# Kernel tuning notes

Hardware: AMD Instinct MI355X
Metric: run time of the kernel (lower is better)

The kernel has to match this reference:

```python
import jax, jax.numpy as jnp
import numpy as np

EPS = 1e-8  # torch CosineSimilarity default eps


def setup_inputs() -> dict:
    key = jax.random.key(0)
    k_emb, k_idx, k_w1, k_w2 = jax.random.split(key, 4)
    N, H, E = 50000, 128, 800000
    emb = jax.random.normal(k_emb, (N, H), dtype=jnp.float32)
    edge_index = jax.random.randint(k_idx, (2, E), 0, N, dtype=jnp.int64)
    # xavier_uniform for square H x H: limit = sqrt(6 / (H + H))
    lim = float(np.sqrt(6.0 / (H + H)))
    W1 = jax.random.uniform(k_w1, (H, H), dtype=jnp.float32, minval=-lim, maxval=lim)
    W2 = jax.random.uniform(k_w2, (H, H), dtype=jnp.float32, minval=-lim, maxval=lim)
    b1 = jnp.zeros((H,), dtype=jnp.float32)
    b2 = jnp.zeros((H,), dtype=jnp.float32)
    return {"emb": emb, "edge_index": edge_index, "W1": W1, "b1": b1, "W2": W2, "b2": b2}


def reference(emb, edge_index, W1, b1, W2, b2):
    col, row = edge_index[0], edge_index[1]

    def mlp(x):  # Linear -> (Dropout: identity at eval) -> ELU -> Linear
        h = jax.nn.elu(x @ W1.T + b1)
        return h @ W2.T + b2

    f1 = mlp(emb[col])  # [E, H]
    f2 = mlp(emb[row])  # [E, H]
    n1 = jnp.maximum(jnp.sqrt(jnp.sum(f1 * f1, axis=1)), EPS)
    n2 = jnp.maximum(jnp.sqrt(jnp.sum(f2 * f2, axis=1)), EPS)
    return jnp.sum(f1 * f2, axis=1) / (n1 * n2)  # [E]
```

## Files before the change

kernel.cpp:

```cpp
#include <hip/hip_runtime.h>
#include <math.h>

#define H 128
#define MROWS 64
#define XS 136

typedef __attribute__((ext_vector_type(8))) short short8;
typedef __attribute__((ext_vector_type(4))) float floatx4;

__device__ __forceinline__ unsigned short f2bf(float f) {
    unsigned u = __float_as_uint(f);
    return (unsigned short)((u + 0x7FFFu + ((u >> 16) & 1u)) >> 16);
}

__global__ void prep_weights(const float* __restrict__ W1,
                             const float* __restrict__ W2,
                             unsigned short* __restrict__ Wbf) {
    int i = blockIdx.x * 256 + threadIdx.x;
    if (i < 16384)       Wbf[i] = f2bf(W1[i]);
    else if (i < 32768)  Wbf[i] = f2bf(W2[i - 16384]);
}

__global__ __launch_bounds__(256, 2) void mlp_mfma(
    const float* __restrict__ emb, const unsigned short* __restrict__ Wbf,
    const float* __restrict__ b1, const float* __restrict__ b2,
    signed char* __restrict__ qtab, float* __restrict__ scl, int N)
{
    __shared__ unsigned short Wl[H * XS];
    __shared__ char dbuf[2 * MROWS * XS * 2];
    __shared__ float invn_s[MROWS];
    __shared__ float amax_s[MROWS];

    unsigned short* xs = (unsigned short*)dbuf;
    unsigned short* hs = xs + MROWS * XS;
    float*          gs = (float*)dbuf;

    const int tid   = threadIdx.x;
    const int wave  = tid >> 6, lane = tid & 63;
    const int quad  = lane >> 4, l15 = lane & 15;
    const int node0 = blockIdx.x * MROWS;

    {
        const float4* src = (const float4*)Wbf;
        #pragma unroll
        for (int i = 0; i < 8; ++i) {
            int cc = i * 256 + tid;
            int row = cc >> 4, c = cc & 15;
            *(float4*)(Wl + row * XS + c * 8) = src[cc];
        }
    }
    #pragma unroll
    for (int i = 0; i < 8; ++i) {
        int flat = i * 1024 + tid * 4;
        int rowl = flat >> 7, col = flat & 127;
        float4 v = make_float4(0.f, 0.f, 0.f, 0.f);
        if (node0 + rowl < N)
            v = *(const float4*)(emb + (size_t)(node0 + rowl) * H + col);
        ushort4 b;
        b.x = f2bf(v.x); b.y = f2bf(v.y); b.z = f2bf(v.z); b.w = f2bf(v.w);
        *(ushort4*)(xs + rowl * XS + col) = b;
    }
    __syncthreads();

    short8 afr[4];
    const int mrow = wave * 16 + l15;

    #pragma unroll
    for (int ks = 0; ks < 4; ++ks)
        afr[ks] = *(const short8*)(xs + mrow * XS + ks * 32 + quad * 8);
    #pragma unroll
    for (int nt = 0; nt < 8; ++nt) {
        floatx4 acc = {0.f, 0.f, 0.f, 0.f};
        #pragma unroll
        for (int ks = 0; ks < 4; ++ks) {
            short8 bfr = *(const short8*)(Wl + (nt * 16 + l15) * XS + ks * 32 + quad * 8);
            acc = __builtin_amdgcn_mfma_f32_16x16x32_bf16(afr[ks], bfr, acc, 0, 0, 0);
        }
        const int col = nt * 16 + l15;
        const float bb = b1[col];
        #pragma unroll
        for (int r = 0; r < 4; ++r) {
            float v = acc[r] + bb;
            v = v > 0.f ? v : (__expf(v) - 1.f);
            hs[(wave * 16 + quad * 4 + r) * XS + col] = f2bf(v);
        }
    }
    __syncthreads();

    {
        const float4* src = (const float4*)(Wbf + 16384);
        #pragma unroll
        for (int i = 0; i < 8; ++i) {
            int cc = i * 256 + tid;
            int row = cc >> 4, c = cc & 15;
            *(float4*)(Wl + row * XS + c * 8) = src[cc];
        }
    }
    __syncthreads();

    #pragma unroll
    for (int ks = 0; ks < 4; ++ks)
        afr[ks] = *(const short8*)(hs + mrow * XS + ks * 32 + quad * 8);
    __syncthreads();

    float sq[4] = {0.f, 0.f, 0.f, 0.f};
    float am[4] = {0.f, 0.f, 0.f, 0.f};
    #pragma unroll
    for (int nt = 0; nt < 8; ++nt) {
        floatx4 acc = {0.f, 0.f, 0.f, 0.f};
        #pragma unroll
        for (int ks = 0; ks < 4; ++ks) {
            short8 bfr = *(const short8*)(Wl + (nt * 16 + l15) * XS + ks * 32 + quad * 8);
            acc = __builtin_amdgcn_mfma_f32_16x16x32_bf16(afr[ks], bfr, acc, 0, 0, 0);
        }
        const int col = nt * 16 + l15;
        const float bb = b2[col];
        #pragma unroll
        for (int r = 0; r < 4; ++r) {
            float v = acc[r] + bb;
            gs[(wave * 16 + quad * 4 + r) * H + col] = v;
            sq[r] += v * v;
            am[r] = fmaxf(am[r], fabsf(v));
        }
    }
    #pragma unroll
    for (int r = 0; r < 4; ++r) {
        float s = sq[r], a = am[r];
        #pragma unroll
        for (int m = 8; m; m >>= 1) {
            s += __shfl_xor(s, m);
            a = fmaxf(a, __shfl_xor(a, m));
        }
        if (l15 == 0) {
            const int row = wave * 16 + quad * 4 + r;
            float nn = sqrtf(s);
            if (nn < 1e-8f) nn = 1e-8f;
            invn_s[row] = 1.f / nn;
            amax_s[row] = fmaxf(a, 1e-20f);
        }
    }
    __syncthreads();

    if (tid < MROWS && node0 + tid < N)
        scl[node0 + tid] = amax_s[tid] * invn_s[tid] * (1.f / 127.f);

    #pragma unroll
    for (int i = 0; i < 2; ++i) {
        int chunk = i * 256 + tid;
        int row = chunk >> 3, c0 = (chunk & 7) * 16;
        if (node0 + row < N) {
            const float qs = 127.f / amax_s[row];
            unsigned u[4];
            #pragma unroll
            for (int w = 0; w < 4; ++w) {
                unsigned pk = 0;
                #pragma unroll
                for (int j = 0; j < 4; ++j) {
                    float v = gs[row * H + c0 + w * 4 + j] * qs;
                    int q = (int)rintf(v);
                    q = q > 127 ? 127 : (q < -127 ? -127 : q);
                    pk |= ((unsigned)(q & 255)) << (8 * j);
                }
                u[w] = pk;
            }
            *(uint4*)(qtab + (size_t)(node0 + row) * H + c0) =
                make_uint4(u[0], u[1], u[2], u[3]);
        }
    }
}

__device__ __forceinline__ int dot4(unsigned a, unsigned b) {
    int s = 0;
    #pragma unroll
    for (int j = 0; j < 4; ++j)
        s += (int)((signed char)(a >> (8 * j))) * (int)((signed char)(b >> (8 * j)));
    return s;
}

__global__ __launch_bounds__(256) void edge_cos(
    const int* __restrict__ ei, const signed char* __restrict__ qtab,
    const float* __restrict__ scl, float* __restrict__ out, int E)
{
    const int gid = blockIdx.x * 256 + threadIdx.x;
    const int e = gid >> 3, sub = gid & 7;
    if (e >= E) return;

    const int c = ei[e];
    const int r = ei[e + E];

    const uint4 ua = *(const uint4*)(qtab + (size_t)c * H + sub * 16);
    const uint4 ub = *(const uint4*)(qtab + (size_t)r * H + sub * 16);
    int s = dot4(ua.x, ub.x) + dot4(ua.y, ub.y)
          + dot4(ua.z, ub.z) + dot4(ua.w, ub.w);

    #pragma unroll
    for (int m = 4; m; m >>= 1) s += __shfl_xor(s, m);
    if (sub == 0) out[e] = (float)s * scl[c] * scl[r];
}

extern "C" void kernel_launch(void* const* d_in, const int* in_sizes, int n_in,
                              void* d_out, int out_size, void* d_ws, size_t ws_size,
                              hipStream_t stream) {
    const float* emb = (const float*)d_in[0];
    const int*   ei  = (const int*)d_in[1];
    const float* W1  = (const float*)d_in[2];
    const float* b1  = (const float*)d_in[3];
    const float* W2  = (const float*)d_in[4];
    const float* b2  = (const float*)d_in[5];
    float*       out = (float*)d_out;

    const int N = in_sizes[0] / H;
    const int E = in_sizes[1] / 2;

    unsigned short* Wbf  = (unsigned short*)d_ws;
    signed char*    qtab = (signed char*)(Wbf + 32768);
    float*          scl  = (float*)(qtab + (size_t)N * H);

    prep_weights<<<128, 256, 0, stream>>>(W1, W2, Wbf);
    mlp_mfma<<<(N + MROWS - 1) / MROWS, 256, 0, stream>>>(emb, Wbf, b1, b2, qtab, scl, N);
    edge_cos<<<(E * 8 + 255) / 256, 256, 0, stream>>>(ei, qtab, scl, out, E);
}
```

Before: 123.5 us.

## Bucket edges by endpoint node range for XCD-local gathers; quantize from registers

Adds histogram, scan and scatter kernels that sort edges into 8x8 buckets by source and destination node range, storing packed (c, r) pairs with the original edge index. The edge kernel then assigns each source bucket to blocks congruent modulo 8, so gathers from the int8 table stay within a smaller slice per cache domain. The MLP epilogue now quantizes directly from accumulator registers instead of staging through shared memory, using a permuted column layout that leaves the dot product unchanged. The cost is extra passes over edge_index, scattered list writes and three more launches, and node ids are packed into 16 bits, which assumes N < 65536.

```diff
diff --git a/kernel.cpp b/kernel.cpp
--- a/kernel.cpp
+++ b/kernel.cpp
@@ -4,6 +4,8 @@
 #define H 128
 #define MROWS 64
 #define XS 136
+#define NB 8
+#define NB2 64
 
 typedef __attribute__((ext_vector_type(8))) short short8;
 typedef __attribute__((ext_vector_type(4))) float floatx4;
@@ -13,12 +15,71 @@
     return (unsigned short)((u + 0x7FFFu + ((u >> 16) & 1u)) >> 16);
 }
 
+__device__ __forceinline__ int bkt(int c, float s8) {
+    int b = (int)((float)c * s8);
+    return b > (NB - 1) ? (NB - 1) : b;
+}
+
 __global__ void prep_weights(const float* __restrict__ W1,
                              const float* __restrict__ W2,
-                             unsigned short* __restrict__ Wbf) {
+                             unsigned short* __restrict__ Wbf,
+                             unsigned* __restrict__ cnt) {
+    if (blockIdx.x == 0 && threadIdx.x < NB2) cnt[threadIdx.x] = 0;
     int i = blockIdx.x * 256 + threadIdx.x;
     if (i < 16384)       Wbf[i] = f2bf(W1[i]);
     else if (i < 32768)  Wbf[i] = f2bf(W2[i - 16384]);
+}
+
+__global__ __launch_bounds__(256) void hist_k(const int* __restrict__ ei, int E,
+                                              float s8, unsigned* __restrict__ cnt) {
+    __shared__ unsigned h[NB2];
+    if (threadIdx.x < NB2) h[threadIdx.x] = 0;
+    __syncthreads();
+    const int stride = gridDim.x * 256;
+    for (int e = blockIdx.x * 256 + threadIdx.x; e < E; e += stride) {
+        int c = ei[e], r = ei[e + E];
+        atomicAdd(&h[bkt(c, s8) * NB + bkt(r, s8)], 1u);
+    }
+    __syncthreads();
+    if (threadIdx.x < NB2 && h[threadIdx.x])
+        atomicAdd(&cnt[threadIdx.x], h[threadIdx.x]);
+}
+
+__global__ void scan_k(const unsigned* __restrict__ cnt,
+                       unsigned* __restrict__ bb, unsigned* __restrict__ cur) {
+    if (threadIdx.x == 0) {
+        unsigned acc = 0;
+        for (int i = 0; i < NB2; ++i) { bb[i] = acc; cur[i] = acc; acc += cnt[i]; }
+        bb[NB2] = acc;
+    }
+}
+
+__global__ __launch_bounds__(256) void scatter_k(const int* __restrict__ ei, int E,
+                                                 float s8, unsigned* __restrict__ cur,
+                                                 uint2* __restrict__ lst) {
+    __shared__ unsigned h[NB2];
+    __shared__ unsigned base_s[NB2];
+    const int nchunk = (E + 255) >> 8;
+    for (int ch = blockIdx.x; ch < nchunk; ch += gridDim.x) {
+        if (threadIdx.x < NB2) h[threadIdx.x] = 0;
+        __syncthreads();
+        const int e = ch * 256 + threadIdx.x;
+        const bool v = e < E;
+        int c = 0, r = 0, b = 0; unsigned rank = 0;
+        if (v) {
+            c = ei[e]; r = ei[e + E];
+            b = bkt(c, s8) * NB + bkt(r, s8);
+            rank = atomicAdd(&h[b], 1u);
+        }
+        __syncthreads();
+        if (threadIdx.x < NB2 && h[threadIdx.x])
+            base_s[threadIdx.x] = atomicAdd(&cur[threadIdx.x], h[threadIdx.x]);
+        __syncthreads();
+        if (v)
+            lst[base_s[b] + rank] =
+                make_uint2((unsigned)c | ((unsigned)r << 16), (unsigned)e);
+        __syncthreads();
+    }
 }
 
 __global__ __launch_bounds__(256, 2) void mlp_mfma(
@@ -27,13 +88,8 @@
     signed char* __restrict__ qtab, float* __restrict__ scl, int N)
 {
     __shared__ unsigned short Wl[H * XS];
-    __shared__ char dbuf[2 * MROWS * XS * 2];
-    __shared__ float invn_s[MROWS];
-    __shared__ float amax_s[MROWS];
-
-    unsigned short* xs = (unsigned short*)dbuf;
-    unsigned short* hs = xs + MROWS * XS;
-    float*          gs = (float*)dbuf;
+    __shared__ unsigned short xs[MROWS * XS];
+    __shared__ unsigned short hs[MROWS * XS];
 
     const int tid   = threadIdx.x;
     const int wave  = tid >> 6, lane = tid & 63;
@@ -62,8 +118,8 @@
     }
     __syncthreads();
 
+    const int mrow = wave * 16 + l15;
     short8 afr[4];
-    const int mrow = wave * 16 + l15;
 
     #pragma unroll
     for (int ks = 0; ks < 4; ++ks)
@@ -77,16 +133,19 @@
             acc = __builtin_amdgcn_mfma_f32_16x16x32_bf16(afr[ks], bfr, acc, 0, 0, 0);
         }
         const int col = nt * 16 + l15;
-        const float bb = b1[col];
+        const float bb1 = b1[col];
         #pragma unroll
         for (int r = 0; r < 4; ++r) {
-            float v = acc[r] + bb;
+            float v = acc[r] + bb1;
             v = v > 0.f ? v : (__expf(v) - 1.f);
             hs[(wave * 16 + quad * 4 + r) * XS + col] = f2bf(v);
         }
     }
     __syncthreads();
 
+    #pragma unroll
+    for (int ks = 0; ks < 4; ++ks)
+        afr[ks] = *(const short8*)(hs + mrow * XS + ks * 32 + quad * 8);
     {
         const float4* src = (const float4*)(Wbf + 16384);
         #pragma unroll
@@ -98,11 +157,7 @@
     }
     __syncthreads();
 
-    #pragma unroll
-    for (int ks = 0; ks < 4; ++ks)
-        afr[ks] = *(const short8*)(hs + mrow * XS + ks * 32 + quad * 8);
-    __syncthreads();
-
+    floatx4 av[8];
     float sq[4] = {0.f, 0.f, 0.f, 0.f};
     float am[4] = {0.f, 0.f, 0.f, 0.f};
     #pragma unroll
@@ -113,12 +168,11 @@
             short8 bfr = *(const short8*)(Wl + (nt * 16 + l15) * XS + ks * 32 + quad * 8);
             acc = __builtin_amdgcn_mfma_f32_16x16x32_bf16(afr[ks], bfr, acc, 0, 0, 0);
         }
-        const int col = nt * 16 + l15;
-        const float bb = b2[col];
+        const float bb2 = b2[nt * 16 + l15];
         #pragma unroll
         for (int r = 0; r < 4; ++r) {
-            float v = acc[r] + bb;
-            gs[(wave * 16 + quad * 4 + r) * H + col] = v;
+            float v = acc[r] + bb2;
+            av[nt][r] = v;
             sq[r] += v * v;
             am[r] = fmaxf(am[r], fabsf(v));
         }
@@ -131,40 +185,34 @@
             s += __shfl_xor(s, m);
             a = fmaxf(a, __shfl_xor(a, m));
         }
-        if (l15 == 0) {
-            const int row = wave * 16 + quad * 4 + r;
-            float nn = sqrtf(s);
-            if (nn < 1e-8f) nn = 1e-8f;
-            invn_s[row] = 1.f / nn;
-            amax_s[row] = fmaxf(a, 1e-20f);
-        }
-    }
-    __syncthreads();
-
-    if (tid < MROWS && node0 + tid < N)
-        scl[node0 + tid] = amax_s[tid] * invn_s[tid] * (1.f / 127.f);
-
-    #pragma unroll
-    for (int i = 0; i < 2; ++i) {
-        int chunk = i * 256 + tid;
-        int row = chunk >> 3, c0 = (chunk & 7) * 16;
-        if (node0 + row < N) {
-            const float qs = 127.f / amax_s[row];
-            unsigned u[4];
+        sq[r] = s; am[r] = a;
+    }
+    #pragma unroll
+    for (int r = 0; r < 4; ++r) {
+        const int row = wave * 16 + quad * 4 + r;
+        const int G = node0 + row;
+        if (G < N) {
+            const float a = fmaxf(am[r], 1e-20f);
+            if (l15 == 0) {
+                float nn = sqrtf(sq[r]);
+                if (nn < 1e-8f) nn = 1e-8f;
+                scl[G] = a / (nn * 127.f);
+            }
+            const float qs = 127.f / a;
+            unsigned pk0 = 0, pk1 = 0;
             #pragma unroll
-            for (int w = 0; w < 4; ++w) {
-                unsigned pk = 0;
-                #pragma unroll
-                for (int j = 0; j < 4; ++j) {
-                    float v = gs[row * H + c0 + w * 4 + j] * qs;
-                    int q = (int)rintf(v);
-                    q = q > 127 ? 127 : (q < -127 ? -127 : q);
-                    pk |= ((unsigned)(q & 255)) << (8 * j);
-                }
-                u[w] = pk;
-            }
-            *(uint4*)(qtab + (size_t)(node0 + row) * H + c0) =
-                make_uint4(u[0], u[1], u[2], u[3]);
+            for (int nt = 0; nt < 4; ++nt) {
+                int q = (int)rintf(av[nt][r] * qs);
+                q = q > 127 ? 127 : (q < -127 ? -127 : q);
+                pk0 |= ((unsigned)(q & 255)) << (8 * nt);
+            }
+            #pragma unroll
+            for (int nt = 4; nt < 8; ++nt) {
+                int q = (int)rintf(av[nt][r] * qs);
+                q = q > 127 ? 127 : (q < -127 ? -127 : q);
+                pk1 |= ((unsigned)(q & 255)) << (8 * (nt - 4));
+            }
+            *(uint2*)(qtab + (size_t)G * H + l15 * 8) = make_uint2(pk0, pk1);
         }
     }
 }
@@ -178,24 +226,37 @@
 }
 
 __global__ __launch_bounds__(256) void edge_cos(
-    const int* __restrict__ ei, const signed char* __restrict__ qtab,
-    const float* __restrict__ scl, float* __restrict__ out, int E)
+    const uint2* __restrict__ lst, const signed char* __restrict__ qtab,
+    const float* __restrict__ scl, const unsigned* __restrict__ bb,
+    float* __restrict__ out)
 {
-    const int gid = blockIdx.x * 256 + threadIdx.x;
-    const int e = gid >> 3, sub = gid & 7;
-    if (e >= E) return;
-
-    const int c = ei[e];
-    const int r = ei[e + E];
-
-    const uint4 ua = *(const uint4*)(qtab + (size_t)c * H + sub * 16);
-    const uint4 ub = *(const uint4*)(qtab + (size_t)r * H + sub * 16);
-    int s = dot4(ua.x, ub.x) + dot4(ua.y, ub.y)
-          + dot4(ua.z, ub.z) + dot4(ua.w, ub.w);
-
-    #pragma unroll
-    for (int m = 4; m; m >>= 1) s += __shfl_xor(s, m);
-    if (sub == 0) out[e] = (float)s * scl[c] * scl[r];
+    const int cb   = blockIdx.x & (NB - 1);
+    const int blk  = blockIdx.x >> 3;
+    const int nblk = gridDim.x >> 3;
+    const unsigned s0 = bb[cb * NB];
+    const unsigned s1 = bb[cb * NB + NB];
+    const int sub  = threadIdx.x & 7;
+    const int slot = threadIdx.x >> 3;
+
+    for (unsigned base = s0 + (unsigned)blk * 32u; base < s1;
+         base += (unsigned)nblk * 32u) {
+        const unsigned idx = base + (unsigned)slot;
+        if (idx < s1) {
+            const uint2 pe = lst[idx];
+            const int c = (int)(pe.x & 0xFFFFu);
+            const int r = (int)(pe.x >> 16);
+            const uint4 ua = *(const uint4*)(qtab + (size_t)c * H + sub * 16);
+            const uint4 ub = *(const uint4*)(qtab + (size_t)r * H + sub * 16);
+            int s = dot4(ua.x, ub.x) + dot4(ua.y, ub.y)
+                  + dot4(ua.z, ub.z) + dot4(ua.w, ub.w);
+            #pragma unroll
+            for (int m = 4; m; m >>= 1) s += __shfl_xor(s, m);
+            if (sub == 0) {
+                float vv = (float)s * scl[c] * scl[r];
+                __builtin_nontemporal_store(vv, out + pe.y);
+            }
+        }
+    }
 }
 
 extern "C" void kernel_launch(void* const* d_in, const int* in_sizes, int n_in,
@@ -214,9 +275,18 @@
 
     unsigned short* Wbf  = (unsigned short*)d_ws;
     signed char*    qtab = (signed char*)(Wbf + 32768);
-    float*          scl  = (float*)(qtab + (size_t)N * H);
-
-    prep_weights<<<128, 256, 0, stream>>>(W1, W2, Wbf);
-    mlp_mfma<<<(N + MROWS - 1) / MROWS, 256, 0, stream>>>(emb, Wbf, b1, b2, qtab, scl, N);
-    edge_cos<<<(E * 8 + 255) / 256, 256, 0, stream>>>(ei, qtab, scl, out, E);
-}
+    float*          sclp = (float*)(qtab + (size_t)N * H);
+    uint2*          lst  = (uint2*)(sclp + N);
+    unsigned*       cnt  = (unsigned*)(lst + E);
+    unsigned*       bb   = cnt + 64;
+    unsigned*       cur  = bb + 72;
+
+    const float s8 = (float)NB / (float)N;
+
+    prep_weights<<<128, 256, 0, stream>>>(W1, W2, Wbf, cnt);
+    hist_k<<<512, 256, 0, stream>>>(ei, E, s8, cnt);
+    scan_k<<<1, 64, 0, stream>>>(cnt, bb, cur);
+    scatter_k<<<1024, 256, 0, stream>>>(ei, E, s8, cur, lst);
+    mlp_mfma<<<(N + MROWS - 1) / MROWS, 256, 0, stream>>>(emb, Wbf, b1, b2, qtab, sclp, N);
+    edge_cos<<<2048, 256, 0, stream>>>(lst, qtab, sclp, bb, out);
+}
```

Result: slower. 182.2 us (+47.5%).

## Keep MLP outputs in registers and batch edges per thread group with sdot4

Applied to the files above, without the earlier changes.

The MLP epilogue now quantizes layer-2 outputs straight from registers instead of staging them through LDS. Each row is written in a permuted column order, which is harmless because only dot products of rows are consumed. The edge kernel has each 8-lane group handle four edges, issuing all index and row gathers up front for more memory-level parallelism. It also uses sdot4 int8 dot instructions and nontemporal loads/stores for the streaming index and output arrays. This raises register pressure in both kernels and removes some LDS syncs.

```diff
diff --git a/kernel.cpp b/kernel.cpp
--- a/kernel.cpp
+++ b/kernel.cpp
@@ -4,6 +4,12 @@
 #define H 128
 #define MROWS 64
 #define XS 136
+
+#if defined(__has_builtin)
+# if __has_builtin(__builtin_amdgcn_sdot4)
+#  define HAVE_SDOT4 1
+# endif
+#endif
 
 typedef __attribute__((ext_vector_type(8))) short short8;
 typedef __attribute__((ext_vector_type(4))) float floatx4;
@@ -27,13 +33,8 @@
     signed char* __restrict__ qtab, float* __restrict__ scl, int N)
 {
     __shared__ unsigned short Wl[H * XS];
-    __shared__ char dbuf[2 * MROWS * XS * 2];
-    __shared__ float invn_s[MROWS];
-    __shared__ float amax_s[MROWS];
-
-    unsigned short* xs = (unsigned short*)dbuf;
-    unsigned short* hs = xs + MROWS * XS;
-    float*          gs = (float*)dbuf;
+    __shared__ unsigned short xs[MROWS * XS];
+    __shared__ unsigned short hs[MROWS * XS];
 
     const int tid   = threadIdx.x;
     const int wave  = tid >> 6, lane = tid & 63;
@@ -62,8 +63,8 @@
     }
     __syncthreads();
 
+    const int mrow = wave * 16 + l15;
     short8 afr[4];
-    const int mrow = wave * 16 + l15;
 
     #pragma unroll
     for (int ks = 0; ks < 4; ++ks)
@@ -77,16 +78,19 @@
             acc = __builtin_amdgcn_mfma_f32_16x16x32_bf16(afr[ks], bfr, acc, 0, 0, 0);
         }
         const int col = nt * 16 + l15;
-        const float bb = b1[col];
+        const float bb1 = b1[col];
         #pragma unroll
         for (int r = 0; r < 4; ++r) {
-            float v = acc[r] + bb;
+            float v = acc[r] + bb1;
             v = v > 0.f ? v : (__expf(v) - 1.f);
             hs[(wave * 16 + quad * 4 + r) * XS + col] = f2bf(v);
         }
     }
     __syncthreads();
 
+    #pragma unroll
+    for (int ks = 0; ks < 4; ++ks)
+        afr[ks] = *(const short8*)(hs + mrow * XS + ks * 32 + quad * 8);
     {
         const float4* src = (const float4*)(Wbf + 16384);
         #pragma unroll
@@ -98,11 +102,7 @@
     }
     __syncthreads();
 
-    #pragma unroll
-    for (int ks = 0; ks < 4; ++ks)
-        afr[ks] = *(const short8*)(hs + mrow * XS + ks * 32 + quad * 8);
-    __syncthreads();
-
+    floatx4 av[8];
     float sq[4] = {0.f, 0.f, 0.f, 0.f};
     float am[4] = {0.f, 0.f, 0.f, 0.f};
     #pragma unroll
@@ -113,12 +113,11 @@
             short8 bfr = *(const short8*)(Wl + (nt * 16 + l15) * XS + ks * 32 + quad * 8);
             acc = __builtin_amdgcn_mfma_f32_16x16x32_bf16(afr[ks], bfr, acc, 0, 0, 0);
         }
-        const int col = nt * 16 + l15;
-        const float bb = b2[col];
+        const float bb2 = b2[nt * 16 + l15];
         #pragma unroll
         for (int r = 0; r < 4; ++r) {
-            float v = acc[r] + bb;
-            gs[(wave * 16 + quad * 4 + r) * H + col] = v;
+            float v = acc[r] + bb2;
+            av[nt][r] = v;
             sq[r] += v * v;
             am[r] = fmaxf(am[r], fabsf(v));
         }
@@ -131,71 +130,95 @@
             s += __shfl_xor(s, m);
             a = fmaxf(a, __shfl_xor(a, m));
         }
-        if (l15 == 0) {
-            const int row = wave * 16 + quad * 4 + r;
-            float nn = sqrtf(s);
-            if (nn < 1e-8f) nn = 1e-8f;
-            invn_s[row] = 1.f / nn;
-            amax_s[row] = fmaxf(a, 1e-20f);
-        }
-    }
-    __syncthreads();
-
-    if (tid < MROWS && node0 + tid < N)
-        scl[node0 + tid] = amax_s[tid] * invn_s[tid] * (1.f / 127.f);
-
-    #pragma unroll
-    for (int i = 0; i < 2; ++i) {
-        int chunk = i * 256 + tid;
-        int row = chunk >> 3, c0 = (chunk & 7) * 16;
-        if (node0 + row < N) {
-            const float qs = 127.f / amax_s[row];
-            unsigned u[4];
+        sq[r] = s; am[r] = a;
+    }
+    #pragma unroll
+    for (int r = 0; r < 4; ++r) {
+        const int row = wave * 16 + quad * 4 + r;
+        const int G = node0 + row;
+        if (G < N) {
+            const float a = fmaxf(am[r], 1e-20f);
+            if (l15 == 0) {
+                float nn = sqrtf(sq[r]);
+                if (nn < 1e-8f) nn = 1e-8f;
+                scl[G] = a / (nn * 127.f);
+            }
+            const float qs = 127.f / a;
+            unsigned pk0 = 0, pk1 = 0;
             #pragma unroll
-            for (int w = 0; w < 4; ++w) {
-                unsigned pk = 0;
-                #pragma unroll
-                for (int j = 0; j < 4; ++j) {
-                    float v = gs[row * H + c0 + w * 4 + j] * qs;
-                    int q = (int)rintf(v);
-                    q = q > 127 ? 127 : (q < -127 ? -127 : q);
-                    pk |= ((unsigned)(q & 255)) << (8 * j);
-                }
-                u[w] = pk;
+            for (int nt = 0; nt < 4; ++nt) {
+                int q = (int)rintf(av[nt][r] * qs);
+                q = q > 127 ? 127 : (q < -127 ? -127 : q);
+                pk0 |= ((unsigned)(q & 255)) << (8 * nt);
             }
-            *(uint4*)(qtab + (size_t)(node0 + row) * H + c0) =
-                make_uint4(u[0], u[1], u[2], u[3]);
-        }
-    }
-}
-
-__device__ __forceinline__ int dot4(unsigned a, unsigned b) {
+            #pragma unroll
+            for (int nt = 4; nt < 8; ++nt) {
+                int q = (int)rintf(av[nt][r] * qs);
+                q = q > 127 ? 127 : (q < -127 ? -127 : q);
+                pk1 |= ((unsigned)(q & 255)) << (8 * (nt - 4));
+            }
+            *(uint2*)(qtab + (size_t)G * H + l15 * 8) = make_uint2(pk0, pk1);
+        }
+    }
+}
+
+__device__ __forceinline__ int dot4s(unsigned a, unsigned b) {
     int s = 0;
     #pragma unroll
     for (int j = 0; j < 4; ++j)
         s += (int)((signed char)(a >> (8 * j))) * (int)((signed char)(b >> (8 * j)));
     return s;
+}
+
+__device__ __forceinline__ int dot16(uint4 a, uint4 b) {
+#if defined(HAVE_SDOT4)
+    int s = __builtin_amdgcn_sdot4((int)a.x, (int)b.x, 0, false);
+    s = __builtin_amdgcn_sdot4((int)a.y, (int)b.y, s, false);
+    s = __builtin_amdgcn_sdot4((int)a.z, (int)b.z, s, false);
+    s = __builtin_amdgcn_sdot4((int)a.w, (int)b.w, s, false);
+    return s;
+#else
+    return dot4s(a.x, b.x) + dot4s(a.y, b.y) + dot4s(a.z, b.z) + dot4s(a.w, b.w);
+#endif
 }
 
 __global__ __launch_bounds__(256) void edge_cos(
     const int* __restrict__ ei, const signed char* __restrict__ qtab,
     const float* __restrict__ scl, float* __restrict__ out, int E)
 {
-    const int gid = blockIdx.x * 256 + threadIdx.x;
-    const int e = gid >> 3, sub = gid & 7;
-    if (e >= E) return;
-
-    const int c = ei[e];
-    const int r = ei[e + E];
-
-    const uint4 ua = *(const uint4*)(qtab + (size_t)c * H + sub * 16);
-    const uint4 ub = *(const uint4*)(qtab + (size_t)r * H + sub * 16);
-    int s = dot4(ua.x, ub.x) + dot4(ua.y, ub.y)
-          + dot4(ua.z, ub.z) + dot4(ua.w, ub.w);
-
-    #pragma unroll
-    for (int m = 4; m; m >>= 1) s += __shfl_xor(s, m);
-    if (sub == 0) out[e] = (float)s * scl[c] * scl[r];
+    const int tid = threadIdx.x;
+    const int sub = tid & 7;
+    const int g   = (blockIdx.x * 256 + tid) >> 3;
+    const int e0  = g * 4;
+    if (e0 >= E) return;
+
+    int cc[4], rr[4];
+    #pragma unroll
+    for (int k = 0; k < 4; ++k) {
+        int e = e0 + k;
+        if (e >= E) e = E - 1;
+        cc[k] = __builtin_nontemporal_load(ei + e);
+        rr[k] = __builtin_nontemporal_load(ei + e + E);
+    }
+    uint4 ua[4], ub[4];
+    #pragma unroll
+    for (int k = 0; k < 4; ++k) {
+        ua[k] = *(const uint4*)(qtab + (size_t)cc[k] * H + sub * 16);
+        ub[k] = *(const uint4*)(qtab + (size_t)rr[k] * H + sub * 16);
+    }
+    float sc[4];
+    #pragma unroll
+    for (int k = 0; k < 4; ++k) sc[k] = scl[cc[k]] * scl[rr[k]];
+
+    #pragma unroll
+    for (int k = 0; k < 4; ++k) {
+        int s = dot16(ua[k], ub[k]);
+        s += __shfl_xor(s, 4);
+        s += __shfl_xor(s, 2);
+        s += __shfl_xor(s, 1);
+        if (sub == 0 && e0 + k < E)
+            __builtin_nontemporal_store((float)s * sc[k], out + e0 + k);
+    }
 }
 
 extern "C" void kernel_launch(void* const* d_in, const int* in_sizes, int n_in,
@@ -214,9 +237,9 @@
 
     unsigned short* Wbf  = (unsigned short*)d_ws;
     signed char*    qtab = (signed char*)(Wbf + 32768);
-    float*          scl  = (float*)(qtab + (size_t)N * H);
+    float*          sclp = (float*)(qtab + (size_t)N * H);
 
     prep_weights<<<128, 256, 0, stream>>>(W1, W2, Wbf);
-    mlp_mfma<<<(N + MROWS - 1) / MROWS, 256, 0, stream>>>(emb, Wbf, b1, b2, qtab, scl, N);
-    edge_cos<<<(E * 8 + 255) / 256, 256, 0, stream>>>(ei, qtab, scl, out, E);
-}
+    mlp_mfma<<<(N + MROWS - 1) / MROWS, 256, 0, stream>>>(emb, Wbf, b1, b2, qtab, sclp, N);
+    edge_cos<<<(E + 127) / 128, 256, 0, stream>>>(ei, qtab, sclp, out, E);
+}
```

After: 121.5 us. Within noise of the previous version (-1.6%).
